# Kernel tuning notes

Measured on AMD Instinct MI355X. Metric: run time of the kernel, lower is better.

Reference implementation:

```python
import jax, jax.numpy as jnp
import numpy as np

HEADS = 8
DIM_HEAD = 128
SCALE = DIM_HEAD ** -0.5
EPS = 1e-5


def layer_norm(t, w, b):
    mu = t.mean(-1, keepdims=True)
    var = ((t - mu) ** 2).mean(-1, keepdims=True)
    return (t - mu) * jax.lax.rsqrt(var + EPS) * w + b


def setup_inputs() -> dict:
    key = jax.random.key(0)
    ks = jax.random.split(key, 8)
    b, n, dim = 4, 1024, 1024
    inner = HEADS * DIM_HEAD  # 1024
    w = 0.02
    return {
        "x": jax.random.normal(ks[0], (b, n, dim), jnp.float32),
        "cond_info": jax.random.normal(ks[1], (b, n, dim), jnp.float32),
        "ref": jax.random.normal(ks[2], (b, n, dim), jnp.float32),
        "ln_w": jnp.ones((dim,), jnp.float32),
        "ln_b": jnp.zeros((dim,), jnp.float32),
        "cln_w": jnp.ones((dim,), jnp.float32),
        "cln_b": jnp.zeros((dim,), jnp.float32),
        "Wk": jax.random.normal(ks[3], (3 * dim, inner), jnp.float32) * w,
        "Wv": jax.random.normal(ks[4], (2 * dim, inner), jnp.float32) * w,
        "Wo": jax.random.normal(ks[5], (inner, dim), jnp.float32) * w,
        "bo": jnp.zeros((dim,), jnp.float32),
        "th_w": jax.random.normal(ks[6], (HEADS, HEADS), jnp.float32) * 0.3,
        "cth_w": jax.random.normal(ks[7], (HEADS, HEADS), jnp.float32) * 0.3,
    }


def reference(x, cond_info, ref, ln_w, ln_b, cln_w, cln_b, Wk, Wv, Wo, bo, th_w, cth_w):
    b, n, _ = x.shape
    h, d = HEADS, DIM_HEAD
    xn = layer_norm(x, ln_w, ln_b)
    rn = layer_norm(ref, ln_w, ln_b)
    cn = layer_norm(cond_info, cln_w, cln_b)
    # projections (y_to_q output is unused in the original forward; omitted)
    cond = jnp.concatenate([xn, cn, rn], axis=-1) @ Wk   # [b, n, h*d]
    refv = jnp.concatenate([xn, rn], axis=-1) @ Wv       # [b, n, h*d]
    split = lambda t: t.reshape(b, n, h, d).transpose(0, 2, 1, 3)  # b h n d
    cond, refv = split(cond), split(refv)
    sim = jnp.einsum('bhid,bhjd->bhij', cond, refv) * SCALE
    attn = jax.nn.softmax(sim, axis=-1)           # row softmax
    context_attn = jax.nn.softmax(sim, axis=-2)   # column softmax
    # talking heads: 1x1 conv over head dim, weight [out_h, in_h]
    attn = jnp.einsum('gh,bhij->bgij', th_w, attn)
    context_attn = jnp.einsum('gh,bhij->bgij', cth_w, context_attn)
    out = jnp.einsum('bhij,bhjd->bhid', attn, refv)
    context_out = jnp.einsum('bhji,bhjd->bhid', context_attn, cond)
    merge = lambda t: t.transpose(0, 2, 1, 3).reshape(b, n, h * d)
    out = merge(out) @ Wo + bo
    context_out = merge(context_out)
    return out, context_out
```

## Files before the change

kernel.cpp:

```cpp
#include <hip/hip_runtime.h>
#include <hip/hip_bf16.h>
#include <stdint.h>

typedef unsigned short u16;
typedef __attribute__((ext_vector_type(8))) short bf16x8;
typedef __attribute__((ext_vector_type(4))) float f32x4;

#define HEADS 8
#define DHEAD 128
#define NSEQ 1024
#define BATCH 4
#define DIM 1024
#define ATT_SCALE 0.088388347648318447f

static __device__ __forceinline__ float bf2f(u16 u){
  union { unsigned int i; float f; } c; c.i = ((unsigned int)u) << 16; return c.f;
}
static __device__ __forceinline__ u16 f2bf(float f){
  union { float f; unsigned int i; } c; c.f = f;
  unsigned int x = c.i;
  return (u16)((x + 0x7fffu + ((x >> 16) & 1u)) >> 16);
}

static __device__ __forceinline__ void gload_lds16(const void* g, void* l){
  __builtin_amdgcn_global_load_lds((__attribute__((address_space(1))) void*)(g),
                                   (__attribute__((address_space(3))) void*)(l),
                                   16, 0, 0);
}

__global__ __launch_bounds__(256)
void ln3_kernel(const float* __restrict__ x, const float* __restrict__ ref,
                const float* __restrict__ cinfo,
                const float* __restrict__ ln_w, const float* __restrict__ ln_b,
                const float* __restrict__ cln_w, const float* __restrict__ cln_b,
                u16* __restrict__ xn, u16* __restrict__ rn, u16* __restrict__ cn)
{
  const int z = blockIdx.y;
  const float* src = (z==0) ? x : (z==1) ? ref : cinfo;
  const float* w   = (z==2) ? cln_w : ln_w;
  const float* b   = (z==2) ? cln_b : ln_b;
  u16* out         = (z==0) ? xn : (z==1) ? rn : cn;

  const int row = blockIdx.x;
  const int t = threadIdx.x;
  const float* xr = src + (size_t)row * DIM;
  float4 v4 = *(const float4*)(xr + t*4);
  float v[4] = {v4.x, v4.y, v4.z, v4.w};
  float s = v[0]+v[1]+v[2]+v[3];
  __shared__ float red[256];
  red[t] = s; __syncthreads();
  for (int o=128;o;o>>=1){ if (t<o) red[t]+=red[t+o]; __syncthreads(); }
  const float mean = red[0] * (1.0f/DIM);
  __syncthreads();
  s = 0.f;
#pragma unroll
  for (int i=0;i<4;i++){ float d = v[i]-mean; s += d*d; }
  red[t] = s; __syncthreads();
  for (int o=128;o;o>>=1){ if (t<o) red[t]+=red[t+o]; __syncthreads(); }
  const float rstd = rsqrtf(red[0]*(1.0f/DIM) + 1e-5f);
  float4 w4 = *(const float4*)(w + t*4);
  float4 b4 = *(const float4*)(b + t*4);
  float wv[4] = {w4.x, w4.y, w4.z, w4.w};
  float bv[4] = {b4.x, b4.y, b4.z, b4.w};
  union { uint2 u; u16 s[4]; } ov;
#pragma unroll
  for (int i=0;i<4;i++)
    ov.s[i] = f2bf((v[i]-mean)*rstd*wv[i] + bv[i]);
  *(uint2*)(out + (size_t)row*DIM + t*4) = ov.u;
}

__global__ __launch_bounds__(256)
void wcvt_kernel(const float* __restrict__ Wk, const float* __restrict__ Wv,
                 const float* __restrict__ Wo,
                 u16* __restrict__ WkT, u16* __restrict__ WvT, u16* __restrict__ WoT)
{
  const int z = blockIdx.z;
  const int K = (z==0) ? 3072 : (z==1) ? 2048 : 1024;
  if ((int)blockIdx.x*32 >= K) return;
  const float* W = (z==0) ? Wk : (z==1) ? Wv : Wo;
  u16* WT = (z==0) ? WkT : (z==1) ? WvT : WoT;
  __shared__ float tile[32][33];
  const int k0 = blockIdx.x*32, n0 = blockIdx.y*32;
  const int t = threadIdx.x, tc = t&31, tr = t>>5;
#pragma unroll
  for (int p=0;p<4;p++)
    tile[tr+p*8][tc] = W[(size_t)(k0+tr+p*8)*DIM + n0+tc];
  __syncthreads();
#pragma unroll
  for (int p=0;p<4;p++)
    WT[(size_t)(n0+tr+p*8)*K + k0+tc] = f2bf(tile[tc][tr+p*8]);
}

template<int BK>
__global__ __launch_bounds__(256)
void gemm_kernel(const u16* __restrict__ A0, const u16* __restrict__ A1,
                 const u16* __restrict__ A2, const u16* __restrict__ A0b,
                 const u16* __restrict__ A1b,
                 const u16* __restrict__ B1, const u16* __restrict__ B2,
                 void* __restrict__ Cv, void* __restrict__ Cv2,
                 const float* __restrict__ bias,
                 int K1, int K2, int lda, int ldb1, int ldb2, int ldc,
                 long a_plane, long b_plane, long c_plane,
                 int epi1, int epi2, int z_split, float alpha)
{
  constexpr int SUBS = BK/32;
  __shared__ __attribute__((aligned(16))) u16 sA[2][SUBS*4096];
  __shared__ __attribute__((aligned(16))) u16 sB[2][SUBS*4096];
  const int t = threadIdx.x;
  const int m0 = blockIdx.y*128, n0 = blockIdx.x*128;
  const int zz = blockIdx.z;
  const bool side = (zz >= z_split);
  const int z = side ? (zz - z_split) : zz;
  const u16* a0 = (side ? A0b : A0) + (size_t)z*a_plane;
  const u16* a1 = (side ? A1b : A1) + (size_t)z*a_plane;
  const u16* a2 = A2 + (size_t)z*a_plane;
  const u16* bB = (side ? B2 : B1) + (size_t)z*b_plane;
  void* Cp = side ? Cv2 : Cv;
  const int EPI = side ? epi2 : epi1;
  const int K   = side ? K2 : K1;
  const int ldb = side ? ldb2 : ldb1;

  const int wave = t>>6, lane = t&63;
  const int wm = (wave>>1)*64, wn = (wave&1)*64;
  const int lm = lane&15, q = lane>>4;

  const f32x4 zero4 = {0.f,0.f,0.f,0.f};
  f32x4 acc[4][4];
#pragma unroll
  for (int i=0;i<4;i++)
#pragma unroll
    for (int j=0;j<4;j++) acc[i][j] = zero4;

  const int arowblk = wave*32;

  const int KT = K / BK;

  auto issueA = [&](int kt, int buf){
    const int kg = kt*BK, seg = kg>>10, ka = kg&1023;
    const u16* Ap = (seg==0) ? a0 : (seg==1 ? a1 : a2);
#pragma unroll
    for (int sub=0; sub<SUBS; ++sub)
#pragma unroll
      for (int rr=0; rr<2; ++rr){
        const int rb = arowblk + rr*16;
        gload_lds16(Ap + (size_t)(m0+rb+lm)*lda + (ka + sub*32 + q*8),
                    &sA[buf][sub*4096 + rb*32]);
      }
  };
  auto issueB = [&](int kt, int buf){
    const int kg = kt*BK;
#pragma unroll
    for (int sub=0; sub<SUBS; ++sub)
#pragma unroll
      for (int rr=0; rr<2; ++rr){
        const int rb = arowblk + rr*16;
        gload_lds16(bB + (size_t)(n0+rb+lm)*ldb + (kg + sub*32 + q*8),
                    &sB[buf][sub*4096 + rb*32]);
      }
  };

  issueA(0, 0);
  issueB(0, 0);

  int cur = 0;
  for (int kt=0; kt<KT; ++kt){
    __syncthreads();
    if (kt+1 < KT){
      issueA(kt+1, cur^1);
      issueB(kt+1, cur^1);
    }
#pragma unroll
    for (int sub=0; sub<SUBS; ++sub){
      bf16x8 af[4], bfr[4];
#pragma unroll
      for (int f=0; f<4; ++f){
        af[f]  = *(const bf16x8*)&sA[cur][sub*4096 + ((wm>>4)+f)*512 + lane*8];
        bfr[f] = *(const bf16x8*)&sB[cur][sub*4096 + ((wn>>4)+f)*512 + lane*8];
      }
#pragma unroll
      for (int fm=0; fm<4; ++fm)
#pragma unroll
        for (int fn=0; fn<4; ++fn)
          acc[fm][fn] = __builtin_amdgcn_mfma_f32_16x16x32_bf16(af[fm], bfr[fn], acc[fm][fn], 0, 0, 0);
    }
    cur ^= 1;
  }

#pragma unroll
  for (int fm=0; fm<4; ++fm){
#pragma unroll
    for (int fn=0; fn<4; ++fn){
#pragma unroll
      for (int r=0; r<4; ++r){
        const int m = m0 + wm + fm*16 + q*4 + r;
        const int n = n0 + wn + fn*16 + lm;
        float val = acc[fm][fn][r] * alpha;
        if (EPI == 0){
          ((u16*)Cp)[(size_t)z*c_plane + (size_t)m*ldc + n] = f2bf(val);
        } else if (EPI == 1){
          ((u16*)Cp)[((size_t)(z>>3)*NSEQ + m)*DIM + (size_t)(z&7)*DHEAD + n] = f2bf(val);
        } else if (EPI == 2){
          ((float*)Cp)[(size_t)m*ldc + n] = val + bias[n];
        } else if (EPI == 3){
          ((u16*)Cp)[(size_t)(((m>>10)*HEADS + (n>>7))*NSEQ + (m&1023))*DHEAD + (n&127)] = f2bf(val);
        } else {
          ((float*)Cp)[((size_t)(z>>3)*NSEQ + m)*DIM + (size_t)(z&7)*DHEAD + n] = val;
        }
      }
    }
  }
}

__global__ __launch_bounds__(256)
void gemmqk_kernel(const u16* __restrict__ cond, const u16* __restrict__ refv,
                   u16* __restrict__ sim,
                   float* __restrict__ RP, float* __restrict__ RS,
                   float* __restrict__ CP, float* __restrict__ CS)
{
  __shared__ __attribute__((aligned(16))) u16 sA[2][4096];
  __shared__ __attribute__((aligned(16))) u16 sB[2][4096];
  const int t = threadIdx.x;
  const int m0 = blockIdx.y*128, n0 = blockIdx.x*128;
  const int z = blockIdx.z;
  const u16* A = cond + (size_t)z*NSEQ*DHEAD;
  const u16* B = refv + (size_t)z*NSEQ*DHEAD;

  const int wave = t>>6, lane = t&63;
  const int wm = (wave>>1)*64, wn = (wave&1)*64;
  const int lm = lane&15, q = lane>>4;

  const f32x4 zero4 = {0.f,0.f,0.f,0.f};
  f32x4 acc[4][4];
#pragma unroll
  for (int i=0;i<4;i++)
#pragma unroll
    for (int j=0;j<4;j++) acc[i][j] = zero4;

  const int arowblk = wave*32;

  auto issueA = [&](int kt, int buf){
    const int kg = kt<<5;
#pragma unroll
    for (int rr=0; rr<2; ++rr){
      const int rb = arowblk + rr*16;
      gload_lds16(A + (size_t)(m0+rb+lm)*DHEAD + (kg + q*8), &sA[buf][rb*32]);
    }
  };
  auto issueB = [&](int kt, int buf){
    const int kg = kt<<5;
#pragma unroll
    for (int rr=0; rr<2; ++rr){
      const int rb = arowblk + rr*16;
      gload_lds16(B + (size_t)(n0+rb+lm)*DHEAD + (kg + q*8), &sB[buf][rb*32]);
    }
  };

  issueA(0, 0); issueB(0, 0);

  int cur = 0;
  for (int kt=0; kt<4; ++kt){
    __syncthreads();
    if (kt+1 < 4){
      issueA(kt+1, cur^1);
      issueB(kt+1, cur^1);
    }
    bf16x8 af[4], bfr[4];
#pragma unroll
    for (int f=0; f<4; ++f){
      af[f]  = *(const bf16x8*)&sA[cur][((wm>>4)+f)*512 + lane*8];
      bfr[f] = *(const bf16x8*)&sB[cur][((wn>>4)+f)*512 + lane*8];
    }
#pragma unroll
    for (int fm=0; fm<4; ++fm)
#pragma unroll
      for (int fn=0; fn<4; ++fn)
        acc[fm][fn] = __builtin_amdgcn_mfma_f32_16x16x32_bf16(af[fm], bfr[fn], acc[fm][fn], 0, 0, 0);
    cur ^= 1;
  }

#pragma unroll
  for (int fm=0; fm<4; ++fm){
#pragma unroll
    for (int fn=0; fn<4; ++fn){
#pragma unroll
      for (int r=0; r<4; ++r){
        const int m = m0 + wm + fm*16 + q*4 + r;
        const int n = n0 + wn + fn*16 + lm;
        const u16 bv = f2bf(acc[fm][fn][r] * ATT_SCALE);
        sim[((size_t)z*NSEQ + m)*NSEQ + n] = bv;
        acc[fm][fn][r] = bf2f(bv);
      }
    }
  }

  const int xg = blockIdx.x*2 + (wn>>6);
#pragma unroll
  for (int fm=0; fm<4; ++fm){
#pragma unroll
    for (int r=0; r<4; ++r){
      float rm = fmaxf(fmaxf(acc[fm][0][r], acc[fm][1][r]),
                       fmaxf(acc[fm][2][r], acc[fm][3][r]));
#pragma unroll
      for (int msk=1; msk<16; msk<<=1) rm = fmaxf(rm, __shfl_xor(rm, msk));
      float rs = __expf(acc[fm][0][r]-rm) + __expf(acc[fm][1][r]-rm)
               + __expf(acc[fm][2][r]-rm) + __expf(acc[fm][3][r]-rm);
#pragma unroll
      for (int msk=1; msk<16; msk<<=1) rs += __shfl_xor(rs, msk);
      if (lm == 0){
        const int m = m0 + wm + fm*16 + q*4 + r;
        RP[((size_t)z*NSEQ + m)*16 + xg] = rm;
        RS[((size_t)z*NSEQ + m)*16 + xg] = rs;
      }
    }
  }

  const int yg = blockIdx.y*2 + (wm>>6);
#pragma unroll
  for (int fn=0; fn<4; ++fn){
    float cm = -1e30f;
#pragma unroll
    for (int fm=0; fm<4; ++fm)
#pragma unroll
      for (int r=0; r<4; ++r) cm = fmaxf(cm, acc[fm][fn][r]);
    cm = fmaxf(cm, __shfl_xor(cm, 16));
    cm = fmaxf(cm, __shfl_xor(cm, 32));
    float cs = 0.f;
#pragma unroll
    for (int fm=0; fm<4; ++fm)
#pragma unroll
      for (int r=0; r<4; ++r) cs += __expf(acc[fm][fn][r]-cm);
    cs += __shfl_xor(cs, 16);
    cs += __shfl_xor(cs, 32);
    if (q == 0){
      const int n = n0 + wn + fn*16 + lm;
      CP[((size_t)z*NSEQ + n)*16 + yg] = cm;
      CS[((size_t)z*NSEQ + n)*16 + yg] = cs;
    }
  }
}

__global__ __launch_bounds__(256)
void redstats_kernel(const float* __restrict__ RP, const float* __restrict__ RS,
                     const float* __restrict__ CP, const float* __restrict__ CS,
                     float* __restrict__ rmax, float* __restrict__ rrcp,
                     float* __restrict__ cmax, float* __restrict__ crcp)
{
  const int gid = blockIdx.x*256 + threadIdx.x;
  const bool isrow = gid < 32768;
  const int item = isrow ? gid : gid - 32768;
  const float* P = isrow ? RP : CP;
  const float* S = isrow ? RS : CS;
  float M = -1e30f;
#pragma unroll
  for (int g=0; g<16; g++) M = fmaxf(M, P[(size_t)item*16 + g]);
  float s = 0.f;
#pragma unroll
  for (int g=0; g<16; g++) s += S[(size_t)item*16 + g] * __expf(P[(size_t)item*16 + g] - M);
  if (isrow){ rmax[item] = M; rrcp[item] = 1.0f/s; }
  else      { cmax[item] = M; crcp[item] = 1.0f/s; }
}

__global__ __launch_bounds__(256)
void gemm8_kernel(const u16* __restrict__ A, const u16* __restrict__ B,
                  float* __restrict__ P)
{
  __shared__ __attribute__((aligned(16))) u16 sA[2][4096];
  __shared__ __attribute__((aligned(16))) u16 sB[2][4096];
  const int t = threadIdx.x;
  const int bid = blockIdx.x;
  const int w = (bid & 7)*128 + (bid >> 3);
  const int x = w & 7;
  const int y = (w >> 3) & 31;
  const int s = w >> 8;
  const int m0 = y*128, n0 = x*128, k0 = s*256;

  const int wave = t>>6, lane = t&63;
  const int wm = (wave>>1)*64, wn = (wave&1)*64;
  const int lm = lane&15, q = lane>>4;

  const f32x4 zero4 = {0.f,0.f,0.f,0.f};
  f32x4 acc[4][4];
#pragma unroll
  for (int i=0;i<4;i++)
#pragma unroll
    for (int j=0;j<4;j++) acc[i][j] = zero4;

  const int arowblk = wave*32;

  auto issueA = [&](int kt, int buf){
    const int kg = k0 + (kt<<5);
#pragma unroll
    for (int rr=0; rr<2; ++rr){
      const int rb = arowblk + rr*16;
      gload_lds16(A + (size_t)(m0+rb+lm)*1024 + (kg + q*8), &sA[buf][rb*32]);
    }
  };
  auto issueB = [&](int kt, int buf){
    const int kg = k0 + (kt<<5);
#pragma unroll
    for (int rr=0; rr<2; ++rr){
      const int rb = arowblk + rr*16;
      gload_lds16(B + (size_t)(n0+rb+lm)*1024 + (kg + q*8), &sB[buf][rb*32]);
    }
  };

  issueA(0, 0); issueB(0, 0);

  int cur = 0;
  for (int kt=0; kt<8; ++kt){
    __syncthreads();
    if (kt+1 < 8){
      issueA(kt+1, cur^1);
      issueB(kt+1, cur^1);
    }
    bf16x8 af[4], bfr[4];
#pragma unroll
    for (int f=0; f<4; ++f){
      af[f]  = *(const bf16x8*)&sA[cur][((wm>>4)+f)*512 + lane*8];
      bfr[f] = *(const bf16x8*)&sB[cur][((wn>>4)+f)*512 + lane*8];
    }
#pragma unroll
    for (int fm=0; fm<4; ++fm)
#pragma unroll
      for (int fn=0; fn<4; ++fn)
        acc[fm][fn] = __builtin_amdgcn_mfma_f32_16x16x32_bf16(af[fm], bfr[fn], acc[fm][fn], 0, 0, 0);
    cur ^= 1;
  }

  float* Pp = P + (size_t)s*4194304;
#pragma unroll
  for (int fm=0; fm<4; ++fm){
#pragma unroll
    for (int fn=0; fn<4; ++fn){
#pragma unroll
      for (int r=0; r<4; ++r){
        const int m = m0 + wm + fm*16 + q*4 + r;
        const int n = n0 + wn + fn*16 + lm;
        Pp[(size_t)m*1024 + n] = acc[fm][fn][r];
      }
    }
  }
}

__global__ __launch_bounds__(256)
void red8_kernel(const float* __restrict__ P, const float* __restrict__ bias,
                 float* __restrict__ out)
{
  const int idx = blockIdx.x*256 + threadIdx.x;
  const float4* P4 = (const float4*)P;
  float4 a = P4[idx];
  float4 b = P4[idx + 1048576];
  float4 c = P4[idx + 2097152];
  float4 d = P4[idx + 3145728];
  float4 bb = ((const float4*)bias)[idx & 255];
  float4 o;
  o.x = a.x + b.x + c.x + d.x + bb.x;
  o.y = a.y + b.y + c.y + d.y + bb.y;
  o.z = a.z + b.z + c.z + d.z + bb.z;
  o.w = a.w + b.w + c.w + d.w + bb.w;
  ((float4*)out)[idx] = o;
}

__global__ __launch_bounds__(256)
void transpose2_kernel(const u16* __restrict__ cond, const u16* __restrict__ refv,
                       u16* __restrict__ condT, u16* __restrict__ refvT)
{
  __shared__ u16 tile[32][33];
  const int zz = blockIdx.z;
  const u16* X = (zz < 32) ? cond : refv;
  u16* XT      = (zz < 32) ? condT : refvT;
  const int z = zz & 31;
  const int i0 = blockIdx.y*32, d0 = blockIdx.x*32;
  const int t = threadIdx.x;
  const int tc = t & 31, tr = t >> 5;
  const u16* Xp = X + (size_t)z*NSEQ*DHEAD;
#pragma unroll
  for (int p=0;p<4;p++){
    int i = tr + p*8;
    tile[i][tc] = Xp[(size_t)(i0+i)*DHEAD + d0 + tc];
  }
  __syncthreads();
  u16* Op = XT + (size_t)z*DHEAD*NSEQ;
#pragma unroll
  for (int p=0;p<4;p++){
    int d = tr + p*8;
    Op[(size_t)(d0+d)*NSEQ + i0 + tc] = tile[tc][d];
  }
}

__global__ __launch_bounds__(256)
void mix_kernel(u16* simam,
                const float* __restrict__ rmax, const float* __restrict__ rrcp,
                const float* __restrict__ cmax, const float* __restrict__ crcp,
                const float* __restrict__ thw, const float* __restrict__ cthw,
                u16* __restrict__ cmT)
{
  __shared__ float s_th[64], s_cth[64];
  __shared__ u16 s_cm[8][32][33];
  const int t = threadIdx.x;
  if (t < 64){ s_th[t] = thw[t]; s_cth[t] = cthw[t]; }
  __syncthreads();
  const int b = blockIdx.z, i0 = blockIdx.y*32, j0 = blockIdx.x*32;
  const int tj = t & 31, ti = t >> 5;
  for (int p=0;p<4;p++){
    const int i = ti + p*8;
    float a[8], c[8];
#pragma unroll
    for (int h=0;h<8;h++){
      const int bh = b*8 + h;
      const float v = bf2f(simam[((size_t)bh*NSEQ + (i0+i))*NSEQ + j0 + tj]);
      a[h] = __expf(v - rmax[(size_t)bh*NSEQ + i0+i]) * rrcp[(size_t)bh*NSEQ + i0+i];
      c[h] = __expf(v - cmax[(size_t)bh*NSEQ + j0+tj]) * crcp[(size_t)bh*NSEQ + j0+tj];
    }
#pragma unroll
    for (int g=0;g<8;g++){
      float sa = 0.f, sc = 0.f;
#pragma unroll
      for (int h=0;h<8;h++){ sa += s_th[g*8+h]*a[h]; sc += s_cth[g*8+h]*c[h]; }
      simam[((size_t)(b*8+g)*NSEQ + (i0+i))*NSEQ + j0 + tj] = f2bf(sa);
      s_cm[g][i][tj] = f2bf(sc);
    }
  }
  __syncthreads();
#pragma unroll
  for (int g=0;g<8;g++){
#pragma unroll
    for (int p=0;p<4;p++){
      const int j = ti + p*8;
      cmT[((size_t)(b*8+g)*NSEQ + (j0+j))*NSEQ + i0 + tj] = s_cm[g][tj][j];
    }
  }
}

extern "C" void kernel_launch(void* const* d_in, const int* in_sizes, int n_in,
                              void* d_out, int out_size, void* d_ws, size_t ws_size,
                              hipStream_t stream)
{
  const float* x     = (const float*)d_in[0];
  const float* cinfo = (const float*)d_in[1];
  const float* ref   = (const float*)d_in[2];
  const float* ln_w  = (const float*)d_in[3];
  const float* ln_b  = (const float*)d_in[4];
  const float* cln_w = (const float*)d_in[5];
  const float* cln_b = (const float*)d_in[6];
  const float* Wk    = (const float*)d_in[7];
  const float* Wv    = (const float*)d_in[8];
  const float* Wo    = (const float*)d_in[9];
  const float* bo    = (const float*)d_in[10];
  const float* thw   = (const float*)d_in[11];
  const float* cthw  = (const float*)d_in[12];
  float* out = (float*)d_out;

  char* ws = (char*)d_ws;
  u16* xn    = (u16*)(ws + 0);
  u16* cn    = (u16*)(ws + 8388608);
  u16* rn    = (u16*)(ws + 16777216);
  u16* cond  = (u16*)(ws + 25165824);
  u16* refv  = (u16*)(ws + 33554432);
  u16* condT = (u16*)(ws + 41943040);
  u16* refvT = (u16*)(ws + 50331648);
  u16* sim   = (u16*)(ws + 58720256);
  u16* cmT   = (u16*)(ws + 125829120);
  u16* WkT   = (u16*)(ws + 192937984);
  u16* WvT   = (u16*)(ws + 199229440);
  u16* WoT   = (u16*)(ws + 203423744);
  float* RP = (float*)(ws + 8388608);
  float* RS = (float*)(ws + 8388608 + 2097152);
  float* CP = (float*)(ws + 8388608 + 4194304);
  float* CS = (float*)(ws + 8388608 + 6291456);
  float* rmax = (float*)(ws + 16777216);
  float* rrcp = (float*)(ws + 16777216 + 131072);
  float* cmax = (float*)(ws + 16777216 + 262144);
  float* crcp = (float*)(ws + 16777216 + 393216);
  u16* out_pre = (u16*)(ws + 0);

  ln3_kernel<<<dim3(4096,3), 256, 0, stream>>>(x, ref, cinfo, ln_w, ln_b,
                                               cln_w, cln_b, xn, rn, cn);

  wcvt_kernel<<<dim3(96,32,3), 256, 0, stream>>>(Wk, Wv, Wo, WkT, WvT, WoT);

  gemm_kernel<64><<<dim3(8,32,2), 256, 0, stream>>>(
      xn, cn, rn, xn, rn, WkT, WvT, cond, refv, nullptr,
      3072, 2048, DIM, 3072, 2048, 0, 0, 0, 0, 3, 3, 1, 1.0f);

  transpose2_kernel<<<dim3(4,32,64), 256, 0, stream>>>(cond, refv, condT, refvT);

  gemmqk_kernel<<<dim3(8,8,32), 256, 0, stream>>>(cond, refv, sim, RP, RS, CP, CS);
  redstats_kernel<<<256, 256, 0, stream>>>(RP, RS, CP, CS, rmax, rrcp, cmax, crcp);

  mix_kernel<<<dim3(32,32,4), 256, 0, stream>>>(sim, rmax, rrcp, cmax, crcp, thw, cthw, cmT);

  gemm_kernel<64><<<dim3(1,8,64), 256, 0, stream>>>(
      sim, sim, sim, cmT, cmT, refvT, condT, out_pre, out + (size_t)BATCH*NSEQ*DIM, nullptr,
      1024, 1024, NSEQ, NSEQ, NSEQ, 0,
      (long)NSEQ*NSEQ, (long)DHEAD*NSEQ, 0, 1, 4, 32, 1.0f);

  gemm8_kernel<<<1024, 256, 0, stream>>>(out_pre, WoT, (float*)sim);
  red8_kernel<<<4096, 256, 0, stream>>>((const float*)sim, bo, out);
}
```

Before: 447.4 us.

## Interleave prefetch loads with MFMA phases in GEMM main loop using setprio

Rewrites the GEMM K-loop into four phases per 64-wide K tile, each loading fragments from LDS, issuing one slice of the next tile's global-to-LDS prefetch, then running 8 MFMAs under raised wave priority with explicit barriers and vmcnt waits. This spreads global loads across the compute instead of issuing them all at the tile start, aiming for better memory/compute overlap in the projection and attention-value GEMMs. It adds many more barriers per iteration, and the hand-tuned vmcnt counts must match the number of outstanding loads exactly.

After: 446.8 us. About the same (-0.1%).

```diff
diff --git a/kernel.cpp b/kernel.cpp
--- a/kernel.cpp
+++ b/kernel.cpp
@@ -91,7 +91,6 @@
     WT[(size_t)(n0+tr+p*8)*K + k0+tc] = f2bf(tile[tc][tr+p*8]);
 }
 
-template<int BK>
 __global__ __launch_bounds__(256)
 void gemm_kernel(const u16* __restrict__ A0, const u16* __restrict__ A1,
                  const u16* __restrict__ A2, const u16* __restrict__ A0b,
@@ -103,9 +102,8 @@
                  long a_plane, long b_plane, long c_plane,
                  int epi1, int epi2, int z_split, float alpha)
 {
-  constexpr int SUBS = BK/32;
-  __shared__ __attribute__((aligned(16))) u16 sA[2][SUBS*4096];
-  __shared__ __attribute__((aligned(16))) u16 sB[2][SUBS*4096];
+  __shared__ __attribute__((aligned(16))) u16 sA[2][8192];
+  __shared__ __attribute__((aligned(16))) u16 sB[2][8192];
   const int t = threadIdx.x;
   const int m0 = blockIdx.y*128, n0 = blockIdx.x*128;
   const int zz = blockIdx.z;
@@ -132,57 +130,117 @@
     for (int j=0;j<4;j++) acc[i][j] = zero4;
 
   const int arowblk = wave*32;
-
-  const int KT = K / BK;
-
-  auto issueA = [&](int kt, int buf){
-    const int kg = kt*BK, seg = kg>>10, ka = kg&1023;
+  const int KT = K >> 6;
+
+  auto issueA2 = [&](int kt, int buf, int sub){
+    const int kg = kt<<6, seg = kg>>10, ka = kg&1023;
     const u16* Ap = (seg==0) ? a0 : (seg==1 ? a1 : a2);
 #pragma unroll
-    for (int sub=0; sub<SUBS; ++sub)
-#pragma unroll
-      for (int rr=0; rr<2; ++rr){
-        const int rb = arowblk + rr*16;
-        gload_lds16(Ap + (size_t)(m0+rb+lm)*lda + (ka + sub*32 + q*8),
-                    &sA[buf][sub*4096 + rb*32]);
-      }
+    for (int rr=0; rr<2; ++rr){
+      const int rb = arowblk + rr*16;
+      gload_lds16(Ap + (size_t)(m0+rb+lm)*lda + (ka + sub*32 + q*8),
+                  &sA[buf][sub*4096 + rb*32]);
+    }
   };
-  auto issueB = [&](int kt, int buf){
-    const int kg = kt*BK;
-#pragma unroll
-    for (int sub=0; sub<SUBS; ++sub)
-#pragma unroll
-      for (int rr=0; rr<2; ++rr){
-        const int rb = arowblk + rr*16;
-        gload_lds16(bB + (size_t)(n0+rb+lm)*ldb + (kg + sub*32 + q*8),
-                    &sB[buf][sub*4096 + rb*32]);
-      }
+  auto issueB2 = [&](int kt, int buf, int sub){
+    const int kg = kt<<6;
+#pragma unroll
+    for (int rr=0; rr<2; ++rr){
+      const int rb = arowblk + rr*16;
+      gload_lds16(bB + (size_t)(n0+rb+lm)*ldb + (kg + sub*32 + q*8),
+                  &sB[buf][sub*4096 + rb*32]);
+    }
   };
 
-  issueA(0, 0);
-  issueB(0, 0);
+  issueA2(0,0,0); issueB2(0,0,0); issueA2(0,0,1); issueB2(0,0,1);
+  asm volatile("s_waitcnt vmcnt(0)" ::: "memory");
+  __builtin_amdgcn_s_barrier();
 
   int cur = 0;
   for (int kt=0; kt<KT; ++kt){
-    __syncthreads();
-    if (kt+1 < KT){
-      issueA(kt+1, cur^1);
-      issueB(kt+1, cur^1);
-    }
-#pragma unroll
-    for (int sub=0; sub<SUBS; ++sub){
-      bf16x8 af[4], bfr[4];
-#pragma unroll
-      for (int f=0; f<4; ++f){
-        af[f]  = *(const bf16x8*)&sA[cur][sub*4096 + ((wm>>4)+f)*512 + lane*8];
-        bfr[f] = *(const bf16x8*)&sB[cur][sub*4096 + ((wn>>4)+f)*512 + lane*8];
-      }
-#pragma unroll
-      for (int fm=0; fm<4; ++fm)
-#pragma unroll
-        for (int fn=0; fn<4; ++fn)
-          acc[fm][fn] = __builtin_amdgcn_mfma_f32_16x16x32_bf16(af[fm], bfr[fn], acc[fm][fn], 0, 0, 0);
-    }
+    const bool pf = (kt+1 < KT);
+    bf16x8 afA, afB, bf0, bf1, bf2, bf3;
+
+    afA = *(const bf16x8*)&sA[cur][((wm>>4)+0)*512 + lane*8];
+    afB = *(const bf16x8*)&sA[cur][((wm>>4)+1)*512 + lane*8];
+    bf0 = *(const bf16x8*)&sB[cur][((wn>>4)+0)*512 + lane*8];
+    bf1 = *(const bf16x8*)&sB[cur][((wn>>4)+1)*512 + lane*8];
+    bf2 = *(const bf16x8*)&sB[cur][((wn>>4)+2)*512 + lane*8];
+    bf3 = *(const bf16x8*)&sB[cur][((wn>>4)+3)*512 + lane*8];
+    if (pf) issueA2(kt+1, cur^1, 0);
+    __builtin_amdgcn_s_barrier();
+    __builtin_amdgcn_s_setprio(1);
+    acc[0][0] = __builtin_amdgcn_mfma_f32_16x16x32_bf16(afA, bf0, acc[0][0], 0,0,0);
+    acc[0][1] = __builtin_amdgcn_mfma_f32_16x16x32_bf16(afA, bf1, acc[0][1], 0,0,0);
+    acc[0][2] = __builtin_amdgcn_mfma_f32_16x16x32_bf16(afA, bf2, acc[0][2], 0,0,0);
+    acc[0][3] = __builtin_amdgcn_mfma_f32_16x16x32_bf16(afA, bf3, acc[0][3], 0,0,0);
+    acc[1][0] = __builtin_amdgcn_mfma_f32_16x16x32_bf16(afB, bf0, acc[1][0], 0,0,0);
+    acc[1][1] = __builtin_amdgcn_mfma_f32_16x16x32_bf16(afB, bf1, acc[1][1], 0,0,0);
+    acc[1][2] = __builtin_amdgcn_mfma_f32_16x16x32_bf16(afB, bf2, acc[1][2], 0,0,0);
+    acc[1][3] = __builtin_amdgcn_mfma_f32_16x16x32_bf16(afB, bf3, acc[1][3], 0,0,0);
+    __builtin_amdgcn_s_setprio(0);
+    __builtin_amdgcn_s_barrier();
+
+    afA = *(const bf16x8*)&sA[cur][((wm>>4)+2)*512 + lane*8];
+    afB = *(const bf16x8*)&sA[cur][((wm>>4)+3)*512 + lane*8];
+    if (pf){
+      issueB2(kt+1, cur^1, 0);
+      asm volatile("s_waitcnt vmcnt(4)" ::: "memory");
+    } else {
+      asm volatile("s_waitcnt vmcnt(0)" ::: "memory");
+    }
+    __builtin_amdgcn_s_barrier();
+    __builtin_amdgcn_s_setprio(1);
+    acc[2][0] = __builtin_amdgcn_mfma_f32_16x16x32_bf16(afA, bf0, acc[2][0], 0,0,0);
+    acc[2][1] = __builtin_amdgcn_mfma_f32_16x16x32_bf16(afA, bf1, acc[2][1], 0,0,0);
+    acc[2][2] = __builtin_amdgcn_mfma_f32_16x16x32_bf16(afA, bf2, acc[2][2], 0,0,0);
+    acc[2][3] = __builtin_amdgcn_mfma_f32_16x16x32_bf16(afA, bf3, acc[2][3], 0,0,0);
+    acc[3][0] = __builtin_amdgcn_mfma_f32_16x16x32_bf16(afB, bf0, acc[3][0], 0,0,0);
+    acc[3][1] = __builtin_amdgcn_mfma_f32_16x16x32_bf16(afB, bf1, acc[3][1], 0,0,0);
+    acc[3][2] = __builtin_amdgcn_mfma_f32_16x16x32_bf16(afB, bf2, acc[3][2], 0,0,0);
+    acc[3][3] = __builtin_amdgcn_mfma_f32_16x16x32_bf16(afB, bf3, acc[3][3], 0,0,0);
+    __builtin_amdgcn_s_setprio(0);
+    __builtin_amdgcn_s_barrier();
+
+    afA = *(const bf16x8*)&sA[cur][4096 + ((wm>>4)+0)*512 + lane*8];
+    afB = *(const bf16x8*)&sA[cur][4096 + ((wm>>4)+1)*512 + lane*8];
+    bf0 = *(const bf16x8*)&sB[cur][4096 + ((wn>>4)+0)*512 + lane*8];
+    bf1 = *(const bf16x8*)&sB[cur][4096 + ((wn>>4)+1)*512 + lane*8];
+    bf2 = *(const bf16x8*)&sB[cur][4096 + ((wn>>4)+2)*512 + lane*8];
+    bf3 = *(const bf16x8*)&sB[cur][4096 + ((wn>>4)+3)*512 + lane*8];
+    if (pf) issueA2(kt+1, cur^1, 1);
+    __builtin_amdgcn_s_barrier();
+    __builtin_amdgcn_s_setprio(1);
+    acc[0][0] = __builtin_amdgcn_mfma_f32_16x16x32_bf16(afA, bf0, acc[0][0], 0,0,0);
+    acc[0][1] = __builtin_amdgcn_mfma_f32_16x16x32_bf16(afA, bf1, acc[0][1], 0,0,0);
+    acc[0][2] = __builtin_amdgcn_mfma_f32_16x16x32_bf16(afA, bf2, acc[0][2], 0,0,0);
+    acc[0][3] = __builtin_amdgcn_mfma_f32_16x16x32_bf16(afA, bf3, acc[0][3], 0,0,0);
+    acc[1][0] = __builtin_amdgcn_mfma_f32_16x16x32_bf16(afB, bf0, acc[1][0], 0,0,0);
+    acc[1][1] = __builtin_amdgcn_mfma_f32_16x16x32_bf16(afB, bf1, acc[1][1], 0,0,0);
+    acc[1][2] = __builtin_amdgcn_mfma_f32_16x16x32_bf16(afB, bf2, acc[1][2], 0,0,0);
+    acc[1][3] = __builtin_amdgcn_mfma_f32_16x16x32_bf16(afB, bf3, acc[1][3], 0,0,0);
+    __builtin_amdgcn_s_setprio(0);
+    __builtin_amdgcn_s_barrier();
+
+    afA = *(const bf16x8*)&sA[cur][4096 + ((wm>>4)+2)*512 + lane*8];
+    afB = *(const bf16x8*)&sA[cur][4096 + ((wm>>4)+3)*512 + lane*8];
+    if (pf){
+      issueB2(kt+1, cur^1, 1);
+      asm volatile("s_waitcnt vmcnt(4)" ::: "memory");
+    }
+    __builtin_amdgcn_s_barrier();
+    __builtin_amdgcn_s_setprio(1);
+    acc[2][0] = __builtin_amdgcn_mfma_f32_16x16x32_bf16(afA, bf0, acc[2][0], 0,0,0);
+    acc[2][1] = __builtin_amdgcn_mfma_f32_16x16x32_bf16(afA, bf1, acc[2][1], 0,0,0);
+    acc[2][2] = __builtin_amdgcn_mfma_f32_16x16x32_bf16(afA, bf2, acc[2][2], 0,0,0);
+    acc[2][3] = __builtin_amdgcn_mfma_f32_16x16x32_bf16(afA, bf3, acc[2][3], 0,0,0);
+    acc[3][0] = __builtin_amdgcn_mfma_f32_16x16x32_bf16(afB, bf0, acc[3][0], 0,0,0);
+    acc[3][1] = __builtin_amdgcn_mfma_f32_16x16x32_bf16(afB, bf1, acc[3][1], 0,0,0);
+    acc[3][2] = __builtin_amdgcn_mfma_f32_16x16x32_bf16(afB, bf2, acc[3][2], 0,0,0);
+    acc[3][3] = __builtin_amdgcn_mfma_f32_16x16x32_bf16(afB, bf3, acc[3][3], 0,0,0);
+    __builtin_amdgcn_s_setprio(0);
+    __builtin_amdgcn_s_barrier();
+
     cur ^= 1;
   }
 
@@ -579,7 +637,7 @@
 
   wcvt_kernel<<<dim3(96,32,3), 256, 0, stream>>>(Wk, Wv, Wo, WkT, WvT, WoT);
 
-  gemm_kernel<64><<<dim3(8,32,2), 256, 0, stream>>>(
+  gemm_kernel<<<dim3(8,32,2), 256, 0, stream>>>(
       xn, cn, rn, xn, rn, WkT, WvT, cond, refv, nullptr,
       3072, 2048, DIM, 3072, 2048, 0, 0, 0, 0, 3, 3, 1, 1.0f);
 
@@ -590,7 +648,7 @@
 
   mix_kernel<<<dim3(32,32,4), 256, 0, stream>>>(sim, rmax, rrcp, cmax, crcp, thw, cthw, cmT);
 
-  gemm_kernel<64><<<dim3(1,8,64), 256, 0, stream>>>(
+  gemm_kernel<<<dim3(1,8,64), 256, 0, stream>>>(
       sim, sim, sim, cmT, cmT, refvT, condT, out_pre, out + (size_t)BATCH*NSEQ*DIM, nullptr,
       1024, 1024, NSEQ, NSEQ, NSEQ, 0,
       (long)NSEQ*NSEQ, (long)DHEAD*NSEQ, 0, 1, 4, 32, 1.0f);
```
